# Optimization experiments

Hardware: AMD Instinct MI355X
Metric: run time of the kernel (lower is better)

Reference implementation:

```python
import jax, jax.numpy as jnp
import numpy as np

N, E, NB, P = 100000, 1600000, 1000, 500000


def gcn_conv(x, edge_index, W, b):
    # PyG GCNConv: add self-loops, symmetric D^-1/2 (A+I) D^-1/2 normalization,
    # linear transform, bias.
    n = x.shape[0]
    loop = jnp.arange(n, dtype=edge_index.dtype)
    src = jnp.concatenate([edge_index[0], loop])
    dst = jnp.concatenate([edge_index[1], loop])
    deg = jax.ops.segment_sum(jnp.ones(src.shape[0], x.dtype), dst, num_segments=n)
    dinv = jnp.where(deg > 0, jax.lax.rsqrt(deg), 0.0)
    norm = dinv[src] * dinv[dst]                       # [E+n]
    xw = x @ W                                          # [n, out]
    out = jax.ops.segment_sum(xw[src] * norm[:, None], dst, num_segments=n)
    return out + b


def setup_inputs() -> dict:
    key = jax.random.key(0)
    ks = jax.random.split(key, 12)
    x = jax.random.normal(ks[0], (N, 27), jnp.float32)
    edge_index = jax.random.randint(ks[1], (2, E), 0, N, dtype=jnp.int32)
    bank = jax.random.normal(ks[2], (NB, 27), jnp.float32)
    node1 = jax.random.randint(ks[3], (P,), 0, N + NB, dtype=jnp.int32)
    node2 = jax.random.randint(ks[4], (P,), 0, N + NB, dtype=jnp.int32)

    def lin(k, fan_in, fan_out):
        s = 1.0 / np.sqrt(fan_in)
        kw, kb = jax.random.split(k)
        W = jax.random.uniform(kw, (fan_in, fan_out), jnp.float32, -s, s)
        b = jax.random.uniform(kb, (fan_out,), jnp.float32, -s, s)
        return W, b

    W1, b1 = lin(ks[5], 27, 60)
    W2, b2 = lin(ks[6], 60, 50)
    Wb, bb = lin(ks[7], 27, 50)
    Wf1, bf1 = lin(ks[8], 100, 40)
    Wf2, bf2 = lin(ks[9], 40, 20)
    Wf3, bf3 = lin(ks[10], 20, 4)
    return dict(x=x, bank=bank, W1=W1, b1=b1, W2=W2, b2=b2, Wb=Wb, bb=bb,
                Wf1=Wf1, bf1=bf1, Wf2=Wf2, bf2=bf2, Wf3=Wf3, bf3=bf3,
                edge_index=edge_index, node1=node1, node2=node2)


def reference(x, bank, W1, b1, W2, b2, Wb, bb, Wf1, bf1, Wf2, bf2, Wf3, bf3,
              edge_index, node1, node2):
    h = gcn_conv(x, edge_index, W1, b1)                 # [N, 60]
    h = gcn_conv(h, edge_index, W2, b2)                 # [N, 50]
    bk = bank @ Wb + bb                                 # [NB, 50]
    allh = jnp.concatenate([h, bk], axis=0)             # [N+NB, 50]
    z = jnp.concatenate([allh[node1], allh[node2]], axis=1)  # [P, 100]
    z = z @ Wf1 + bf1
    z = z @ Wf2 + bf2
    z = z @ Wf3 + bf3                                   # [P, 4]
    return jax.nn.softmax(z, axis=0)                    # softmax over dim 0, as in source
```

## Files before the change

kernel.cpp:

```cpp
#include <hip/hip_runtime.h>
#include <math.h>

#define N_NODES 100000
#define N_EDGES 1600000
#define NB_BANK 1000
#define N_PAIRS 500000

#define BUCK_SHIFT 9
#define BUCK_NODES 512
#define NBUCK 196
#define BCAP 10240
#define EPB 4096
#define NSCAT 391
#define NZBLK 1954
#define SMASK 0x1FFFF

struct Consts {
  float C[27*8];
  float Rb[27*8];
  float u[8];
  float vg[8];
  float vb[8];
};

__device__ void precompute_body(
    const float* __restrict__ W1, const float* __restrict__ b1,
    const float* __restrict__ W2, const float* __restrict__ b2,
    const float* __restrict__ Wb, const float* __restrict__ bb,
    const float* __restrict__ Wf1, const float* __restrict__ bf1,
    const float* __restrict__ Wf2, const float* __restrict__ bf2,
    const float* __restrict__ Wf3, const float* __restrict__ bf3,
    Consts* __restrict__ cst) {
  __shared__ float A[40*4];
  __shared__ float T[100*4];
  __shared__ float B[60*8];
  __shared__ float cvec[4];
  const int tid = threadIdx.x;
  const int nt = blockDim.x;

  for (int idx = tid; idx < 160; idx += nt) {
    int r = idx >> 2, k = idx & 3;
    float s = 0.f;
    for (int j = 0; j < 20; ++j) s += Wf2[r*20+j] * Wf3[j*4+k];
    A[idx] = s;
  }
  __syncthreads();
  for (int idx = tid; idx < 400; idx += nt) {
    int r = idx >> 2, k = idx & 3;
    float s = 0.f;
    for (int j = 0; j < 40; ++j) s += Wf1[r*40+j] * A[j*4+k];
    T[idx] = s;
  }
  if (tid < 4) {
    float s = bf3[tid];
    for (int j = 0; j < 40; ++j) s += bf1[j] * A[j*4+tid];
    for (int j = 0; j < 20; ++j) s += bf2[j] * Wf3[j*4+tid];
    cvec[tid] = s;
  }
  __syncthreads();
  for (int idx = tid; idx < 480; idx += nt) {
    int r = idx >> 3, k = idx & 7;
    int half = k >> 2, kk = k & 3;
    float s = 0.f;
    for (int j = 0; j < 50; ++j) s += W2[r*50+j] * T[(half*50+j)*4+kk];
    B[idx] = s;
  }
  __syncthreads();
  for (int idx = tid; idx < 456; idx += nt) {
    if (idx < 216) {
      int r = idx >> 3, k = idx & 7;
      float s = 0.f;
      for (int j = 0; j < 60; ++j) s += W1[r*60+j] * B[j*8+k];
      cst->C[idx] = s;
    } else if (idx < 432) {
      int i2 = idx - 216;
      int r = i2 >> 3, k = i2 & 7, half = k >> 2, kk = k & 3;
      float s = 0.f;
      for (int j = 0; j < 50; ++j) s += Wb[r*50+j] * T[(half*50+j)*4+kk];
      cst->Rb[i2] = s;
    } else if (idx < 440) {
      int k = idx - 432;
      float s = 0.f;
      for (int j = 0; j < 60; ++j) s += b1[j] * B[j*8+k];
      cst->u[k] = s;
    } else if (idx < 448) {
      int k = idx - 440, half = k >> 2, kk = k & 3;
      float s = (half == 0) ? cvec[kk] : 0.f;
      for (int j = 0; j < 50; ++j) s += b2[j] * T[(half*50+j)*4+kk];
      cst->vg[k] = s;
    } else {
      int k = idx - 448, half = k >> 2, kk = k & 3;
      float s = (half == 0) ? cvec[kk] : 0.f;
      for (int j = 0; j < 50; ++j) s += bb[j] * T[(half*50+j)*4+kk];
      cst->vb[k] = s;
    }
  }
}

__global__ __launch_bounds__(1024) void k_scatter(
    const int* __restrict__ ei, int* __restrict__ bcnt, int* __restrict__ ebuf,
    const float* __restrict__ W1, const float* __restrict__ b1,
    const float* __restrict__ W2, const float* __restrict__ b2,
    const float* __restrict__ Wb, const float* __restrict__ bb,
    const float* __restrict__ Wf1, const float* __restrict__ bf1,
    const float* __restrict__ Wf2, const float* __restrict__ bf2,
    const float* __restrict__ Wf3, const float* __restrict__ bf3,
    Consts* __restrict__ cst) {
  if (blockIdx.x == NSCAT) {
    precompute_body(W1, b1, W2, b2, Wb, bb, Wf1, bf1, Wf2, bf2, Wf3, bf3, cst);
    return;
  }
  __shared__ int hist[NBUCK];
  __shared__ int base[NBUCK];
  const int t = threadIdx.x;
  const int e0 = blockIdx.x * EPB;
  int dcache[EPB / 1024];
  if (t < NBUCK) hist[t] = 0;
  __syncthreads();
#pragma unroll
  for (int i = 0; i < EPB / 1024; ++i) {
    int e = e0 + i * 1024 + t;
    int d = (e < N_EDGES) ? ei[N_EDGES + e] : -1;
    dcache[i] = d;
    if (d >= 0) atomicAdd(&hist[d >> BUCK_SHIFT], 1);
  }
  __syncthreads();
  if (t < NBUCK) {
    int h = hist[t];
    base[t] = h ? (t * BCAP + atomicAdd(&bcnt[t], h)) : 0;
    hist[t] = 0;
  }
  __syncthreads();
#pragma unroll
  for (int i = 0; i < EPB / 1024; ++i) {
    int e = e0 + i * 1024 + t;
    int d = dcache[i];
    if (d >= 0) {
      int s = ei[e];
      int b = d >> BUCK_SHIFT;
      int pos = base[b] + atomicAdd(&hist[b], 1);
      ebuf[pos] = ((d & (BUCK_NODES - 1)) << 17) | s;
    }
  }
}

__global__ __launch_bounds__(1024) void k_degfill(const int* __restrict__ bcnt,
                                                  const int* __restrict__ ebuf,
                                                  float* __restrict__ dinv,
                                                  int* __restrict__ rbeg,
                                                  int* __restrict__ rend,
                                                  int* __restrict__ csr) {
  __shared__ int cnt[BUCK_NODES];
  __shared__ int lcur[BUCK_NODES];
  const int b = blockIdx.x;
  const int t = threadIdx.x;
  if (t < BUCK_NODES) cnt[t] = 0;
  __syncthreads();
  const int beg = b * BCAP, end = beg + bcnt[b];
  for (int j = beg + t; j < end; j += 1024)
    atomicAdd(&cnt[ebuf[j] >> 17], 1);
  __syncthreads();
  int v = (t < BUCK_NODES) ? cnt[t] : 0;
  for (int off = 1; off < BUCK_NODES; off <<= 1) {
    int u = (t < BUCK_NODES && t >= off) ? cnt[t - off] : 0;
    __syncthreads();
    if (t < BUCK_NODES) cnt[t] += u;
    __syncthreads();
  }
  if (t < BUCK_NODES) {
    const int node = (b << BUCK_SHIFT) + t;
    const int excl = beg + cnt[t] - v;
    lcur[t] = excl;
    if (node < N_NODES) {
      rbeg[node] = excl;
      rend[node] = excl + v;
      dinv[node] = rsqrtf((float)v + 1.0f);
    }
  }
  __syncthreads();
  for (int j = beg + t; j < end; j += 1024) {
    int code = ebuf[j];
    int pos = atomicAdd(&lcur[code >> 17], 1);
    csr[pos] = code & SMASK;
  }
}

__global__ __launch_bounds__(256) void k_x8(const float* __restrict__ x,
                                            const float* __restrict__ dinv,
                                            const Consts* __restrict__ cst,
                                            float* __restrict__ Xs) {
  __shared__ float xs[32*27];
  const int tid = threadIdx.x;
  const int base = blockIdx.x * 32 * 27;
  for (int j = tid; j < 32*27; j += 256) {
    int g = base + j;
    xs[j] = (g < N_NODES*27) ? x[g] : 0.f;
  }
  __syncthreads();
  int li = tid >> 3, k = tid & 7;
  int node = blockIdx.x * 32 + li;
  if (node < N_NODES) {
    float s = 0.f;
    for (int c = 0; c < 27; ++c) s += xs[li*27+c] * cst->C[c*8+k];
    Xs[node*8+k] = s * dinv[node];
  }
}

__global__ __launch_bounds__(256) void k_gather1(const int* __restrict__ rbeg,
                                                 const int* __restrict__ rend,
                                                 const int* __restrict__ csr,
                                                 const float* __restrict__ dinv,
                                                 const float2* __restrict__ Xs2,
                                                 float2* __restrict__ Ys2,
                                                 float* __restrict__ dvec) {
  int t = blockIdx.x * 256 + threadIdx.x;
  int d = t >> 2, q = t & 3;
  if (d >= N_NODES) return;
  const int beg = rbeg[d], end = rend[d];
  const float nd = dinv[d];
  float2 self = Xs2[d*4 + q];
  float ax = self.x, ay = self.y;
  float dsum = nd;
  int j = beg;
  for (; j + 8 <= end; j += 8) {
    int s0 = csr[j],   s1 = csr[j+1], s2 = csr[j+2], s3 = csr[j+3];
    int s4 = csr[j+4], s5 = csr[j+5], s6 = csr[j+6], s7 = csr[j+7];
    float2 a0 = Xs2[s0*4+q], a1 = Xs2[s1*4+q], a2 = Xs2[s2*4+q], a3 = Xs2[s3*4+q];
    float2 a4 = Xs2[s4*4+q], a5 = Xs2[s5*4+q], a6 = Xs2[s6*4+q], a7 = Xs2[s7*4+q];
    ax += ((a0.x + a1.x) + (a2.x + a3.x)) + ((a4.x + a5.x) + (a6.x + a7.x));
    ay += ((a0.y + a1.y) + (a2.y + a3.y)) + ((a4.y + a5.y) + (a6.y + a7.y));
    if (q == 0)
      dsum += ((dinv[s0] + dinv[s1]) + (dinv[s2] + dinv[s3]))
            + ((dinv[s4] + dinv[s5]) + (dinv[s6] + dinv[s7]));
  }
  for (; j < end; ++j) {
    int s = csr[j];
    float2 a = Xs2[s*4+q];
    ax += a.x; ay += a.y;
    if (q == 0) dsum += dinv[s];
  }
  float nn = nd * nd;
  Ys2[t] = make_float2(nn * ax, nn * ay);
  if (q == 0) dvec[d] = nd * dsum;
}

__global__ __launch_bounds__(256) void k_gather2g(const int* __restrict__ rbeg,
                                                  const int* __restrict__ rend,
                                                  const int* __restrict__ csr,
                                                  const float* __restrict__ dinv,
                                                  const float2* __restrict__ Ys2,
                                                  const float* __restrict__ dvec,
                                                  const float* __restrict__ bank,
                                                  const Consts* __restrict__ cst,
                                                  float2* __restrict__ gall2) {
  int t = blockIdx.x * 256 + threadIdx.x;
  int d = t >> 2, q = t & 3;
  if (d >= N_NODES + NB_BANK) return;
  int c0 = 2*q, c1 = 2*q + 1;
  if (d >= N_NODES) {
    int bk = d - N_NODES;
    float sx = cst->vb[c0], sy = cst->vb[c1];
    for (int cc = 0; cc < 27; ++cc) {
      float bv = bank[bk*27+cc];
      sx += bv * cst->Rb[cc*8+c0];
      sy += bv * cst->Rb[cc*8+c1];
    }
    gall2[t] = make_float2(sx, sy);
    return;
  }
  const int beg = rbeg[d], end = rend[d];
  float2 self = Ys2[d*4 + q];
  float ax = self.x, ay = self.y;
  int j = beg;
  for (; j + 8 <= end; j += 8) {
    int s0 = csr[j],   s1 = csr[j+1], s2 = csr[j+2], s3 = csr[j+3];
    int s4 = csr[j+4], s5 = csr[j+5], s6 = csr[j+6], s7 = csr[j+7];
    float2 a0 = Ys2[s0*4+q], a1 = Ys2[s1*4+q], a2 = Ys2[s2*4+q], a3 = Ys2[s3*4+q];
    float2 a4 = Ys2[s4*4+q], a5 = Ys2[s5*4+q], a6 = Ys2[s6*4+q], a7 = Ys2[s7*4+q];
    ax += ((a0.x + a1.x) + (a2.x + a3.x)) + ((a4.x + a5.x) + (a6.x + a7.x));
    ay += ((a0.y + a1.y) + (a2.y + a3.y)) + ((a4.y + a5.y) + (a6.y + a7.y));
  }
  for (; j < end; ++j) {
    float2 a = Ys2[csr[j]*4+q];
    ax += a.x; ay += a.y;
  }
  float nd = dinv[d], dv = dvec[d];
  gall2[t] = make_float2(nd * ax + dv * cst->u[c0] + cst->vg[c0],
                         nd * ay + dv * cst->u[c1] + cst->vg[c1]);
}

__device__ inline void sm_merge(float4& m1, float4& s1,
                                const float4 m2, const float4 s2) {
  float4 M;
  M.x = fmaxf(m1.x, m2.x); M.y = fmaxf(m1.y, m2.y);
  M.z = fmaxf(m1.z, m2.z); M.w = fmaxf(m1.w, m2.w);
  s1.x = s1.x * expf(m1.x - M.x) + s2.x * expf(m2.x - M.x);
  s1.y = s1.y * expf(m1.y - M.y) + s2.y * expf(m2.y - M.y);
  s1.z = s1.z * expf(m1.z - M.z) + s2.z * expf(m2.z - M.z);
  s1.w = s1.w * expf(m1.w - M.w) + s2.w * expf(m2.w - M.w);
  m1 = M;
}

__global__ __launch_bounds__(256) void k_z(const int* __restrict__ node1,
                                           const int* __restrict__ node2,
                                           const float* __restrict__ gall,
                                           float* __restrict__ z,
                                           float4* __restrict__ bs_m,
                                           float4* __restrict__ bs_s) {
  int p = blockIdx.x * 256 + threadIdx.x;
  float4 m = make_float4(-1e30f, -1e30f, -1e30f, -1e30f);
  float4 s = make_float4(0.f, 0.f, 0.f, 0.f);
  if (p < N_PAIRS) {
    int n1 = node1[p], n2 = node2[p];
    const float4 a = *(const float4*)(gall + (size_t)n1*8);
    const float4 b = *(const float4*)(gall + (size_t)n2*8 + 4);
    float4 zv = make_float4(a.x+b.x, a.y+b.y, a.z+b.z, a.w+b.w);
    ((float4*)z)[p] = zv;
    m = zv; s = make_float4(1.f, 1.f, 1.f, 1.f);
  }
  __shared__ float4 lm[256], ls[256];
  lm[threadIdx.x] = m; ls[threadIdx.x] = s;
  __syncthreads();
  for (int st = 128; st > 0; st >>= 1) {
    if (threadIdx.x < st) {
      float4 mm = lm[threadIdx.x], ss = ls[threadIdx.x];
      sm_merge(mm, ss, lm[threadIdx.x + st], ls[threadIdx.x + st]);
      lm[threadIdx.x] = mm; ls[threadIdx.x] = ss;
    }
    __syncthreads();
  }
  if (threadIdx.x == 0) { bs_m[blockIdx.x] = lm[0]; bs_s[blockIdx.x] = ls[0]; }
}

__global__ __launch_bounds__(256) void k_comb(const float4* __restrict__ bs_m,
                                              const float4* __restrict__ bs_s,
                                              float* __restrict__ gms) {
  float4 m = make_float4(-1e30f, -1e30f, -1e30f, -1e30f);
  float4 s = make_float4(0.f, 0.f, 0.f, 0.f);
  for (int i = threadIdx.x; i < NZBLK; i += 256)
    sm_merge(m, s, bs_m[i], bs_s[i]);
  __shared__ float4 lm[256], ls[256];
  lm[threadIdx.x] = m; ls[threadIdx.x] = s;
  __syncthreads();
  for (int st = 128; st > 0; st >>= 1) {
    if (threadIdx.x < st) {
      float4 mm = lm[threadIdx.x], ss = ls[threadIdx.x];
      sm_merge(mm, ss, lm[threadIdx.x + st], ls[threadIdx.x + st]);
      lm[threadIdx.x] = mm; ls[threadIdx.x] = ss;
    }
    __syncthreads();
  }
  if (threadIdx.x == 0) {
    float4 M = lm[0], S = ls[0];
    gms[0] = M.x; gms[1] = M.y; gms[2] = M.z; gms[3] = M.w;
    gms[4] = S.x; gms[5] = S.y; gms[6] = S.z; gms[7] = S.w;
  }
}

__global__ __launch_bounds__(256) void k_final(const float* __restrict__ z,
                                               const float* __restrict__ gms,
                                               float* __restrict__ out) {
  int p = blockIdx.x * 256 + threadIdx.x;
  if (p < N_PAIRS) {
    float m0 = gms[0], m1 = gms[1], m2 = gms[2], m3 = gms[3];
    float i0 = 1.f / gms[4], i1 = 1.f / gms[5];
    float i2 = 1.f / gms[6], i3 = 1.f / gms[7];
    float4 zv = ((const float4*)z)[p];
    float4 o = make_float4(expf(zv.x - m0) * i0, expf(zv.y - m1) * i1,
                           expf(zv.z - m2) * i2, expf(zv.w - m3) * i3);
    ((float4*)out)[p] = o;
  }
}

extern "C" void kernel_launch(void* const* d_in, const int* in_sizes, int n_in,
                              void* d_out, int out_size, void* d_ws, size_t ws_size,
                              hipStream_t stream) {
  const float* x    = (const float*)d_in[0];
  const float* bank = (const float*)d_in[1];
  const float* W1   = (const float*)d_in[2];
  const float* b1   = (const float*)d_in[3];
  const float* W2   = (const float*)d_in[4];
  const float* b2   = (const float*)d_in[5];
  const float* Wb   = (const float*)d_in[6];
  const float* bb   = (const float*)d_in[7];
  const float* Wf1  = (const float*)d_in[8];
  const float* bf1  = (const float*)d_in[9];
  const float* Wf2  = (const float*)d_in[10];
  const float* bf2  = (const float*)d_in[11];
  const float* Wf3  = (const float*)d_in[12];
  const float* bf3  = (const float*)d_in[13];
  const int* ei     = (const int*)d_in[14];
  const int* node1  = (const int*)d_in[15];
  const int* node2  = (const int*)d_in[16];
  float* out = (float*)d_out;

  char* w = (char*)d_ws;
  size_t off = 0;
  auto take = [&](size_t bytes) -> char* {
    char* p = w + off;
    off = (off + bytes + 255) & ~(size_t)255;
    return p;
  };
  Consts* cst    = (Consts*)take(sizeof(Consts));
  int*    bcnt   = (int*)take(NBUCK * 4);
  float*  dinv   = (float*)take(N_NODES * 4);
  int*    rbeg   = (int*)take(N_NODES * 4);
  int*    rend   = (int*)take(N_NODES * 4);
  int*    csr    = (int*)take((size_t)NBUCK * BCAP * 4);
  float*  Xs     = (float*)take((size_t)N_NODES * 8 * 4);
  float*  Ys     = (float*)take((size_t)N_NODES * 8 * 4);
  float*  dvec   = (float*)take(N_NODES * 4);
  float*  gall   = (float*)take((size_t)(N_NODES + NB_BANK) * 8 * 4);
  char*   shreg  = take((size_t)NBUCK * BCAP * 4 > (size_t)N_PAIRS * 16
                        ? (size_t)NBUCK * BCAP * 4 : (size_t)N_PAIRS * 16);
  int*    ebuf   = (int*)shreg;
  float*  z      = (float*)shreg;
  float4* bs_m   = (float4*)take((size_t)NZBLK * 16);
  float4* bs_s   = (float4*)take((size_t)NZBLK * 16);
  float*  gms    = (float*)take(32);

  hipMemsetAsync(bcnt, 0, NBUCK * 4, stream);

  k_scatter<<<NSCAT + 1, 1024, 0, stream>>>(ei, bcnt, ebuf, W1, b1, W2, b2,
                                            Wb, bb, Wf1, bf1, Wf2, bf2,
                                            Wf3, bf3, cst);
  k_degfill<<<NBUCK, 1024, 0, stream>>>(bcnt, ebuf, dinv, rbeg, rend, csr);
  k_x8<<<(N_NODES + 31) / 32, 256, 0, stream>>>(x, dinv, cst, Xs);
  k_gather1<<<(N_NODES * 4 + 255) / 256, 256, 0, stream>>>(
      rbeg, rend, csr, dinv, (const float2*)Xs, (float2*)Ys, dvec);
  k_gather2g<<<((N_NODES + NB_BANK) * 4 + 255) / 256, 256, 0, stream>>>(
      rbeg, rend, csr, dinv, (const float2*)Ys, dvec, bank, cst, (float2*)gall);
  k_z<<<NZBLK, 256, 0, stream>>>(node1, node2, gall, z, bs_m, bs_s);
  k_comb<<<1, 256, 0, stream>>>(bs_m, bs_s, gms);
  k_final<<<NZBLK, 256, 0, stream>>>(z, gms, out);
}
```

Baseline: 202.7 us.

## Fuse x8 into degfill, float4 split gathers, last-block softmax combine, nontemporal loads

Folds the per-node x·C projection into the degree/CSR-fill kernel, reusing the bucket's in-shared dinv, and folds the single-block softmax combine into k_z through a last-block ticket. This removes two launches. Both gather kernels now have each thread load float4 halves, with two threads splitting the edge list and reducing through a shuffle. Tail edges are padded to a dummy zero node N_NODES, which avoids the scalar remainder loop. Nontemporal loads and stores are added on streaming data. The cost is a 13.8K-float shared buffer per degfill block, which may lower occupancy, plus extra padded loads on short rows.

```diff
diff --git a/kernel.cpp b/kernel.cpp
--- a/kernel.cpp
+++ b/kernel.cpp
@@ -14,6 +14,8 @@
 #define NSCAT 391
 #define NZBLK 1954
 #define SMASK 0x1FFFF
+
+typedef __attribute__((ext_vector_type(4))) float f4raw;
 
 struct Consts {
   float C[27*8];
@@ -120,7 +122,8 @@
 #pragma unroll
   for (int i = 0; i < EPB / 1024; ++i) {
     int e = e0 + i * 1024 + t;
-    int d = (e < N_EDGES) ? ei[N_EDGES + e] : -1;
+    int d = -1;
+    if (e < N_EDGES) d = __builtin_nontemporal_load(&ei[N_EDGES + e]);
     dcache[i] = d;
     if (d >= 0) atomicAdd(&hist[d >> BUCK_SHIFT], 1);
   }
@@ -136,7 +139,7 @@
     int e = e0 + i * 1024 + t;
     int d = dcache[i];
     if (d >= 0) {
-      int s = ei[e];
+      int s = __builtin_nontemporal_load(&ei[e]);
       int b = d >> BUCK_SHIFT;
       int pos = base[b] + atomicAdd(&hist[b], 1);
       ebuf[pos] = ((d & (BUCK_NODES - 1)) << 17) | s;
@@ -144,14 +147,15 @@
   }
 }
 
-__global__ __launch_bounds__(1024) void k_degfill(const int* __restrict__ bcnt,
-                                                  const int* __restrict__ ebuf,
-                                                  float* __restrict__ dinv,
-                                                  int* __restrict__ rbeg,
-                                                  int* __restrict__ rend,
-                                                  int* __restrict__ csr) {
+__global__ __launch_bounds__(1024) void k_degfill_x8(
+    const int* __restrict__ bcnt, const int* __restrict__ ebuf,
+    const float* __restrict__ x, const Consts* __restrict__ cst,
+    float* __restrict__ dinv, int* __restrict__ rbeg, int* __restrict__ rend,
+    int* __restrict__ csr, float* __restrict__ Xs) {
   __shared__ int cnt[BUCK_NODES];
   __shared__ int lcur[BUCK_NODES];
+  __shared__ float sdinv[BUCK_NODES];
+  __shared__ float xs[BUCK_NODES * 27];
   const int b = blockIdx.x;
   const int t = threadIdx.x;
   if (t < BUCK_NODES) cnt[t] = 0;
@@ -159,6 +163,11 @@
   const int beg = b * BCAP, end = beg + bcnt[b];
   for (int j = beg + t; j < end; j += 1024)
     atomicAdd(&cnt[ebuf[j] >> 17], 1);
+  const int xbase = b * (BUCK_NODES * 27);
+  for (int j = t; j < BUCK_NODES * 27; j += 1024) {
+    int g = xbase + j;
+    xs[j] = (g < N_NODES * 27) ? __builtin_nontemporal_load(&x[g]) : 0.f;
+  }
   __syncthreads();
   int v = (t < BUCK_NODES) ? cnt[t] : 0;
   for (int off = 1; off < BUCK_NODES; off <<= 1) {
@@ -171,10 +180,14 @@
     const int node = (b << BUCK_SHIFT) + t;
     const int excl = beg + cnt[t] - v;
     lcur[t] = excl;
+    float dv = (node < N_NODES) ? rsqrtf((float)v + 1.0f) : 0.f;
+    sdinv[t] = dv;
     if (node < N_NODES) {
       rbeg[node] = excl;
       rend[node] = excl + v;
-      dinv[node] = rsqrtf((float)v + 1.0f);
+      dinv[node] = dv;
+    } else if (node == N_NODES) {
+      dinv[node] = 0.f;
     }
   }
   __syncthreads();
@@ -183,110 +196,142 @@
     int pos = atomicAdd(&lcur[code >> 17], 1);
     csr[pos] = code & SMASK;
   }
-}
-
-__global__ __launch_bounds__(256) void k_x8(const float* __restrict__ x,
-                                            const float* __restrict__ dinv,
-                                            const Consts* __restrict__ cst,
-                                            float* __restrict__ Xs) {
-  __shared__ float xs[32*27];
-  const int tid = threadIdx.x;
-  const int base = blockIdx.x * 32 * 27;
-  for (int j = tid; j < 32*27; j += 256) {
-    int g = base + j;
-    xs[j] = (g < N_NODES*27) ? x[g] : 0.f;
-  }
-  __syncthreads();
-  int li = tid >> 3, k = tid & 7;
-  int node = blockIdx.x * 32 + li;
-  if (node < N_NODES) {
-    float s = 0.f;
-    for (int c = 0; c < 27; ++c) s += xs[li*27+c] * cst->C[c*8+k];
-    Xs[node*8+k] = s * dinv[node];
-  }
-}
-
-__global__ __launch_bounds__(256) void k_gather1(const int* __restrict__ rbeg,
-                                                 const int* __restrict__ rend,
-                                                 const int* __restrict__ csr,
-                                                 const float* __restrict__ dinv,
-                                                 const float2* __restrict__ Xs2,
-                                                 float2* __restrict__ Ys2,
-                                                 float* __restrict__ dvec) {
+  for (int idx = t; idx < BUCK_NODES * 8; idx += 1024) {
+    int li = idx >> 3, k = idx & 7;
+    int node = (b << BUCK_SHIFT) + li;
+    if (node <= N_NODES) {
+      float s = 0.f;
+      for (int c = 0; c < 27; ++c) s += xs[li*27+c] * cst->C[c*8+k];
+      Xs[(size_t)node*8+k] = s * sdinv[li];
+    }
+  }
+}
+
+__global__ __launch_bounds__(256) void k_gather1(
+    const int* __restrict__ rbeg, const int* __restrict__ rend,
+    const int* __restrict__ csr, const float* __restrict__ dinv,
+    const float4* __restrict__ Xs4, float4* __restrict__ Ys4,
+    float* __restrict__ dvec) {
   int t = blockIdx.x * 256 + threadIdx.x;
-  int d = t >> 2, q = t & 3;
-  if (d >= N_NODES) return;
-  const int beg = rbeg[d], end = rend[d];
+  int d = t >> 2;
+  if (d > N_NODES) return;
+  int q = t & 1, r = (t >> 1) & 1;
+  if (d == N_NODES) {
+    if (r == 0) Ys4[(size_t)d*2+q] = make_float4(0.f, 0.f, 0.f, 0.f);
+    return;
+  }
+  const int beg = rbeg[d], end = rend[d], e1 = end - 1;
   const float nd = dinv[d];
-  float2 self = Xs2[d*4 + q];
-  float ax = self.x, ay = self.y;
-  float dsum = nd;
-  int j = beg;
-  for (; j + 8 <= end; j += 8) {
-    int s0 = csr[j],   s1 = csr[j+1], s2 = csr[j+2], s3 = csr[j+3];
-    int s4 = csr[j+4], s5 = csr[j+5], s6 = csr[j+6], s7 = csr[j+7];
-    float2 a0 = Xs2[s0*4+q], a1 = Xs2[s1*4+q], a2 = Xs2[s2*4+q], a3 = Xs2[s3*4+q];
-    float2 a4 = Xs2[s4*4+q], a5 = Xs2[s5*4+q], a6 = Xs2[s6*4+q], a7 = Xs2[s7*4+q];
-    ax += ((a0.x + a1.x) + (a2.x + a3.x)) + ((a4.x + a5.x) + (a6.x + a7.x));
-    ay += ((a0.y + a1.y) + (a2.y + a3.y)) + ((a4.y + a5.y) + (a6.y + a7.y));
+  float ax = 0.f, ay = 0.f, az = 0.f, aw = 0.f, dsum = 0.f;
+  for (int j = beg + r; j < end; j += 16) {
+    int k1 = j+2, k2 = j+4, k3 = j+6, k4 = j+8, k5 = j+10, k6 = j+12, k7 = j+14;
+    int c0 = __builtin_nontemporal_load(&csr[j]);
+    int c1 = __builtin_nontemporal_load(&csr[k1 < e1 ? k1 : e1]);
+    int c2 = __builtin_nontemporal_load(&csr[k2 < e1 ? k2 : e1]);
+    int c3 = __builtin_nontemporal_load(&csr[k3 < e1 ? k3 : e1]);
+    int c4 = __builtin_nontemporal_load(&csr[k4 < e1 ? k4 : e1]);
+    int c5 = __builtin_nontemporal_load(&csr[k5 < e1 ? k5 : e1]);
+    int c6 = __builtin_nontemporal_load(&csr[k6 < e1 ? k6 : e1]);
+    int c7 = __builtin_nontemporal_load(&csr[k7 < e1 ? k7 : e1]);
+    int s0 = c0;
+    int s1 = (k1 < end) ? c1 : N_NODES;
+    int s2 = (k2 < end) ? c2 : N_NODES;
+    int s3 = (k3 < end) ? c3 : N_NODES;
+    int s4 = (k4 < end) ? c4 : N_NODES;
+    int s5 = (k5 < end) ? c5 : N_NODES;
+    int s6 = (k6 < end) ? c6 : N_NODES;
+    int s7 = (k7 < end) ? c7 : N_NODES;
+    float4 a0 = Xs4[(size_t)s0*2+q], a1 = Xs4[(size_t)s1*2+q];
+    float4 a2 = Xs4[(size_t)s2*2+q], a3 = Xs4[(size_t)s3*2+q];
+    float4 a4 = Xs4[(size_t)s4*2+q], a5 = Xs4[(size_t)s5*2+q];
+    float4 a6 = Xs4[(size_t)s6*2+q], a7 = Xs4[(size_t)s7*2+q];
+    ax += ((a0.x+a1.x)+(a2.x+a3.x)) + ((a4.x+a5.x)+(a6.x+a7.x));
+    ay += ((a0.y+a1.y)+(a2.y+a3.y)) + ((a4.y+a5.y)+(a6.y+a7.y));
+    az += ((a0.z+a1.z)+(a2.z+a3.z)) + ((a4.z+a5.z)+(a6.z+a7.z));
+    aw += ((a0.w+a1.w)+(a2.w+a3.w)) + ((a4.w+a5.w)+(a6.w+a7.w));
     if (q == 0)
-      dsum += ((dinv[s0] + dinv[s1]) + (dinv[s2] + dinv[s3]))
-            + ((dinv[s4] + dinv[s5]) + (dinv[s6] + dinv[s7]));
-  }
-  for (; j < end; ++j) {
-    int s = csr[j];
-    float2 a = Xs2[s*4+q];
-    ax += a.x; ay += a.y;
-    if (q == 0) dsum += dinv[s];
-  }
-  float nn = nd * nd;
-  Ys2[t] = make_float2(nn * ax, nn * ay);
-  if (q == 0) dvec[d] = nd * dsum;
-}
-
-__global__ __launch_bounds__(256) void k_gather2g(const int* __restrict__ rbeg,
-                                                  const int* __restrict__ rend,
-                                                  const int* __restrict__ csr,
-                                                  const float* __restrict__ dinv,
-                                                  const float2* __restrict__ Ys2,
-                                                  const float* __restrict__ dvec,
-                                                  const float* __restrict__ bank,
-                                                  const Consts* __restrict__ cst,
-                                                  float2* __restrict__ gall2) {
+      dsum += ((dinv[s0]+dinv[s1]) + (dinv[s2]+dinv[s3]))
+            + ((dinv[s4]+dinv[s5]) + (dinv[s6]+dinv[s7]));
+  }
+  ax += __shfl_xor(ax, 2); ay += __shfl_xor(ay, 2);
+  az += __shfl_xor(az, 2); aw += __shfl_xor(aw, 2);
+  if (q == 0) dsum += __shfl_xor(dsum, 2);
+  if (r == 0) {
+    float4 self = Xs4[(size_t)d*2+q];
+    float nn = nd * nd;
+    Ys4[(size_t)d*2+q] = make_float4(nn*(ax+self.x), nn*(ay+self.y),
+                                     nn*(az+self.z), nn*(aw+self.w));
+    if (q == 0) dvec[d] = nd * (dsum + nd);
+  }
+}
+
+__global__ __launch_bounds__(256) void k_gather2g(
+    const int* __restrict__ rbeg, const int* __restrict__ rend,
+    const int* __restrict__ csr, const float* __restrict__ dinv,
+    const float4* __restrict__ Ys4, const float* __restrict__ dvec,
+    const float* __restrict__ bank, const Consts* __restrict__ cst,
+    float4* __restrict__ gall4) {
   int t = blockIdx.x * 256 + threadIdx.x;
-  int d = t >> 2, q = t & 3;
+  int d = t >> 2;
   if (d >= N_NODES + NB_BANK) return;
-  int c0 = 2*q, c1 = 2*q + 1;
+  int q = t & 1, r = (t >> 1) & 1;
   if (d >= N_NODES) {
+    if (r) return;
     int bk = d - N_NODES;
-    float sx = cst->vb[c0], sy = cst->vb[c1];
+    int c0 = 4*q;
+    float sa = cst->vb[c0],   sb = cst->vb[c0+1];
+    float sc = cst->vb[c0+2], sd = cst->vb[c0+3];
     for (int cc = 0; cc < 27; ++cc) {
       float bv = bank[bk*27+cc];
-      sx += bv * cst->Rb[cc*8+c0];
-      sy += bv * cst->Rb[cc*8+c1];
-    }
-    gall2[t] = make_float2(sx, sy);
+      sa += bv * cst->Rb[cc*8+c0];
+      sb += bv * cst->Rb[cc*8+c0+1];
+      sc += bv * cst->Rb[cc*8+c0+2];
+      sd += bv * cst->Rb[cc*8+c0+3];
+    }
+    gall4[(size_t)d*2+q] = make_float4(sa, sb, sc, sd);
     return;
   }
-  const int beg = rbeg[d], end = rend[d];
-  float2 self = Ys2[d*4 + q];
-  float ax = self.x, ay = self.y;
-  int j = beg;
-  for (; j + 8 <= end; j += 8) {
-    int s0 = csr[j],   s1 = csr[j+1], s2 = csr[j+2], s3 = csr[j+3];
-    int s4 = csr[j+4], s5 = csr[j+5], s6 = csr[j+6], s7 = csr[j+7];
-    float2 a0 = Ys2[s0*4+q], a1 = Ys2[s1*4+q], a2 = Ys2[s2*4+q], a3 = Ys2[s3*4+q];
-    float2 a4 = Ys2[s4*4+q], a5 = Ys2[s5*4+q], a6 = Ys2[s6*4+q], a7 = Ys2[s7*4+q];
-    ax += ((a0.x + a1.x) + (a2.x + a3.x)) + ((a4.x + a5.x) + (a6.x + a7.x));
-    ay += ((a0.y + a1.y) + (a2.y + a3.y)) + ((a4.y + a5.y) + (a6.y + a7.y));
-  }
-  for (; j < end; ++j) {
-    float2 a = Ys2[csr[j]*4+q];
-    ax += a.x; ay += a.y;
-  }
-  float nd = dinv[d], dv = dvec[d];
-  gall2[t] = make_float2(nd * ax + dv * cst->u[c0] + cst->vg[c0],
-                         nd * ay + dv * cst->u[c1] + cst->vg[c1]);
+  const int beg = rbeg[d], end = rend[d], e1 = end - 1;
+  float ax = 0.f, ay = 0.f, az = 0.f, aw = 0.f;
+  for (int j = beg + r; j < end; j += 16) {
+    int k1 = j+2, k2 = j+4, k3 = j+6, k4 = j+8, k5 = j+10, k6 = j+12, k7 = j+14;
+    int c0 = __builtin_nontemporal_load(&csr[j]);
+    int c1 = __builtin_nontemporal_load(&csr[k1 < e1 ? k1 : e1]);
+    int c2 = __builtin_nontemporal_load(&csr[k2 < e1 ? k2 : e1]);
+    int c3 = __builtin_nontemporal_load(&csr[k3 < e1 ? k3 : e1]);
+    int c4 = __builtin_nontemporal_load(&csr[k4 < e1 ? k4 : e1]);
+    int c5 = __builtin_nontemporal_load(&csr[k5 < e1 ? k5 : e1]);
+    int c6 = __builtin_nontemporal_load(&csr[k6 < e1 ? k6 : e1]);
+    int c7 = __builtin_nontemporal_load(&csr[k7 < e1 ? k7 : e1]);
+    int s0 = c0;
+    int s1 = (k1 < end) ? c1 : N_NODES;
+    int s2 = (k2 < end) ? c2 : N_NODES;
+    int s3 = (k3 < end) ? c3 : N_NODES;
+    int s4 = (k4 < end) ? c4 : N_NODES;
+    int s5 = (k5 < end) ? c5 : N_NODES;
+    int s6 = (k6 < end) ? c6 : N_NODES;
+    int s7 = (k7 < end) ? c7 : N_NODES;
+    float4 a0 = Ys4[(size_t)s0*2+q], a1 = Ys4[(size_t)s1*2+q];
+    float4 a2 = Ys4[(size_t)s2*2+q], a3 = Ys4[(size_t)s3*2+q];
+    float4 a4 = Ys4[(size_t)s4*2+q], a5 = Ys4[(size_t)s5*2+q];
+    float4 a6 = Ys4[(size_t)s6*2+q], a7 = Ys4[(size_t)s7*2+q];
+    ax += ((a0.x+a1.x)+(a2.x+a3.x)) + ((a4.x+a5.x)+(a6.x+a7.x));
+    ay += ((a0.y+a1.y)+(a2.y+a3.y)) + ((a4.y+a5.y)+(a6.y+a7.y));
+    az += ((a0.z+a1.z)+(a2.z+a3.z)) + ((a4.z+a5.z)+(a6.z+a7.z));
+    aw += ((a0.w+a1.w)+(a2.w+a3.w)) + ((a4.w+a5.w)+(a6.w+a7.w));
+  }
+  ax += __shfl_xor(ax, 2); ay += __shfl_xor(ay, 2);
+  az += __shfl_xor(az, 2); aw += __shfl_xor(aw, 2);
+  if (r == 0) {
+    float4 self = Ys4[(size_t)d*2+q];
+    float nd = dinv[d], dv = dvec[d];
+    int c0 = 4*q;
+    gall4[(size_t)d*2+q] = make_float4(
+        nd*(ax+self.x) + dv*cst->u[c0]   + cst->vg[c0],
+        nd*(ay+self.y) + dv*cst->u[c0+1] + cst->vg[c0+1],
+        nd*(az+self.z) + dv*cst->u[c0+2] + cst->vg[c0+2],
+        nd*(aw+self.w) + dv*cst->u[c0+3] + cst->vg[c0+3]);
+  }
 }
 
 __device__ inline void sm_merge(float4& m1, float4& s1,
@@ -306,19 +351,24 @@
                                            const float* __restrict__ gall,
                                            float* __restrict__ z,
                                            float4* __restrict__ bs_m,
-                                           float4* __restrict__ bs_s) {
+                                           float4* __restrict__ bs_s,
+                                           int* __restrict__ ticket,
+                                           float* __restrict__ gms) {
   int p = blockIdx.x * 256 + threadIdx.x;
   float4 m = make_float4(-1e30f, -1e30f, -1e30f, -1e30f);
   float4 s = make_float4(0.f, 0.f, 0.f, 0.f);
   if (p < N_PAIRS) {
-    int n1 = node1[p], n2 = node2[p];
+    int n1 = __builtin_nontemporal_load(&node1[p]);
+    int n2 = __builtin_nontemporal_load(&node2[p]);
     const float4 a = *(const float4*)(gall + (size_t)n1*8);
     const float4 b = *(const float4*)(gall + (size_t)n2*8 + 4);
     float4 zv = make_float4(a.x+b.x, a.y+b.y, a.z+b.z, a.w+b.w);
-    ((float4*)z)[p] = zv;
+    f4raw zr = {zv.x, zv.y, zv.z, zv.w};
+    __builtin_nontemporal_store(zr, (f4raw*)z + p);
     m = zv; s = make_float4(1.f, 1.f, 1.f, 1.f);
   }
   __shared__ float4 lm[256], ls[256];
+  __shared__ int islast;
   lm[threadIdx.x] = m; ls[threadIdx.x] = s;
   __syncthreads();
   for (int st = 128; st > 0; st >>= 1) {
@@ -329,18 +379,19 @@
     }
     __syncthreads();
   }
-  if (threadIdx.x == 0) { bs_m[blockIdx.x] = lm[0]; bs_s[blockIdx.x] = ls[0]; }
-}
-
-__global__ __launch_bounds__(256) void k_comb(const float4* __restrict__ bs_m,
-                                              const float4* __restrict__ bs_s,
-                                              float* __restrict__ gms) {
-  float4 m = make_float4(-1e30f, -1e30f, -1e30f, -1e30f);
-  float4 s = make_float4(0.f, 0.f, 0.f, 0.f);
+  if (threadIdx.x == 0) {
+    bs_m[blockIdx.x] = lm[0]; bs_s[blockIdx.x] = ls[0];
+    __threadfence();
+    islast = (atomicAdd(ticket, 1) == NZBLK - 1);
+  }
+  __syncthreads();
+  if (!islast) return;
+  __threadfence();
+  float4 m2 = make_float4(-1e30f, -1e30f, -1e30f, -1e30f);
+  float4 s2 = make_float4(0.f, 0.f, 0.f, 0.f);
   for (int i = threadIdx.x; i < NZBLK; i += 256)
-    sm_merge(m, s, bs_m[i], bs_s[i]);
-  __shared__ float4 lm[256], ls[256];
-  lm[threadIdx.x] = m; ls[threadIdx.x] = s;
+    sm_merge(m2, s2, bs_m[i], bs_s[i]);
+  lm[threadIdx.x] = m2; ls[threadIdx.x] = s2;
   __syncthreads();
   for (int st = 128; st > 0; st >>= 1) {
     if (threadIdx.x < st) {
@@ -365,10 +416,10 @@
     float m0 = gms[0], m1 = gms[1], m2 = gms[2], m3 = gms[3];
     float i0 = 1.f / gms[4], i1 = 1.f / gms[5];
     float i2 = 1.f / gms[6], i3 = 1.f / gms[7];
-    float4 zv = ((const float4*)z)[p];
-    float4 o = make_float4(expf(zv.x - m0) * i0, expf(zv.y - m1) * i1,
-                           expf(zv.z - m2) * i2, expf(zv.w - m3) * i3);
-    ((float4*)out)[p] = o;
+    f4raw zv = __builtin_nontemporal_load((const f4raw*)z + p);
+    f4raw o = {expf(zv.x - m0) * i0, expf(zv.y - m1) * i1,
+               expf(zv.z - m2) * i2, expf(zv.w - m3) * i3};
+    __builtin_nontemporal_store(o, (f4raw*)out + p);
   }
 }
 
@@ -402,13 +453,14 @@
     return p;
   };
   Consts* cst    = (Consts*)take(sizeof(Consts));
-  int*    bcnt   = (int*)take(NBUCK * 4);
-  float*  dinv   = (float*)take(N_NODES * 4);
+  int*    bcnt   = (int*)take((NBUCK + 1) * 4);
+  int*    ticket = bcnt + NBUCK;
+  float*  dinv   = (float*)take((N_NODES + 1) * 4);
   int*    rbeg   = (int*)take(N_NODES * 4);
   int*    rend   = (int*)take(N_NODES * 4);
   int*    csr    = (int*)take((size_t)NBUCK * BCAP * 4);
-  float*  Xs     = (float*)take((size_t)N_NODES * 8 * 4);
-  float*  Ys     = (float*)take((size_t)N_NODES * 8 * 4);
+  float*  Xs     = (float*)take((size_t)(N_NODES + 1) * 8 * 4);
+  float*  Ys     = (float*)take((size_t)(N_NODES + 1) * 8 * 4);
   float*  dvec   = (float*)take(N_NODES * 4);
   float*  gall   = (float*)take((size_t)(N_NODES + NB_BANK) * 8 * 4);
   char*   shreg  = take((size_t)NBUCK * BCAP * 4 > (size_t)N_PAIRS * 16
@@ -419,18 +471,17 @@
   float4* bs_s   = (float4*)take((size_t)NZBLK * 16);
   float*  gms    = (float*)take(32);
 
-  hipMemsetAsync(bcnt, 0, NBUCK * 4, stream);
+  hipMemsetAsync(bcnt, 0, (NBUCK + 1) * 4, stream);
 
   k_scatter<<<NSCAT + 1, 1024, 0, stream>>>(ei, bcnt, ebuf, W1, b1, W2, b2,
                                             Wb, bb, Wf1, bf1, Wf2, bf2,
                                             Wf3, bf3, cst);
-  k_degfill<<<NBUCK, 1024, 0, stream>>>(bcnt, ebuf, dinv, rbeg, rend, csr);
-  k_x8<<<(N_NODES + 31) / 32, 256, 0, stream>>>(x, dinv, cst, Xs);
-  k_gather1<<<(N_NODES * 4 + 255) / 256, 256, 0, stream>>>(
-      rbeg, rend, csr, dinv, (const float2*)Xs, (float2*)Ys, dvec);
+  k_degfill_x8<<<NBUCK, 1024, 0, stream>>>(bcnt, ebuf, x, cst,
+                                           dinv, rbeg, rend, csr, Xs);
+  k_gather1<<<((N_NODES + 1) * 4 + 255) / 256, 256, 0, stream>>>(
+      rbeg, rend, csr, dinv, (const float4*)Xs, (float4*)Ys, dvec);
   k_gather2g<<<((N_NODES + NB_BANK) * 4 + 255) / 256, 256, 0, stream>>>(
-      rbeg, rend, csr, dinv, (const float2*)Ys, dvec, bank, cst, (float2*)gall);
-  k_z<<<NZBLK, 256, 0, stream>>>(node1, node2, gall, z, bs_m, bs_s);
-  k_comb<<<1, 256, 0, stream>>>(bs_m, bs_s, gms);
+      rbeg, rend, csr, dinv, (const float4*)Ys, dvec, bank, cst, (float4*)gall);
+  k_z<<<NZBLK, 256, 0, stream>>>(node1, node2, gall, z, bs_m, bs_s, ticket, gms);
   k_final<<<NZBLK, 256, 0, stream>>>(z, gms, out);
 }
```

After: 254.8 us. 1.26x slower.
